# Kernel optimization log

Hardware: AMD Instinct MI355X
Metric: run time of the kernel (lower is better)

## Reference

```python
import jax, jax.numpy as jnp
import numpy as np

BATCH = 256
B_TYPES = 32   # input capsule types
C_TYPES = 10   # output capsule types
H, W = 8, 8    # input spatial extent == kernel (output is 1x1)
POSE = 16      # capsule pose length (shape (16,1))
NUM_ITER = 3
EPS = 1e-8


def setup_inputs() -> dict:
    key = jax.random.key(0)
    k1, k2, k3 = jax.random.split(key, 3)
    input_caps_poses = jax.random.normal(k1, (BATCH, B_TYPES, H, W, POSE, 1), jnp.float32)
    input_caps_activations = jax.random.uniform(k2, (BATCH, B_TYPES, H, W), jnp.float32)
    # nn.init.normal_(std=0.1) on [B, kh, kw, C, os0, is0]
    weight = 0.1 * jax.random.normal(k3, (B_TYPES, H, W, C_TYPES, POSE, POSE), jnp.float32)
    # routing_bias initialized to 0.1: [C, oh, ow, os0, os1]
    routing_bias = jnp.full((C_TYPES, 1, 1, POSE, 1), 0.1, jnp.float32)
    return {
        "input_caps_poses": input_caps_poses,
        "input_caps_activations": input_caps_activations,
        "weight": weight,
        "routing_bias": routing_bias,
    }


def _squash(s):
    # Hinton squash: ||s||^2/(1+||s||^2) * s/||s||, norm over pose dims
    n2 = jnp.sum(s * s, axis=(-2, -1), keepdims=True)
    return (n2 / (1.0 + n2)) * s * jax.lax.rsqrt(n2 + EPS)


def reference(input_caps_poses, input_caps_activations, weight, routing_bias):
    b = input_caps_poses.shape[0]
    # votes[b,c,B,h,w,o,p] = sum_i W[B,h,w,c,o,i] * pose[b,B,h,w,i,p]
    votes = jnp.einsum('Bhwcoi,bBhwip->bcBhwop', weight, input_caps_poses)
    logits = jnp.zeros((b, C_TYPES, B_TYPES, H, W), votes.dtype)
    bias = routing_bias.reshape(1, C_TYPES, POSE, 1)
    v = None
    for it in range(NUM_ITER):
        # coupling coefficients: softmax over output capsule types
        c = jax.nn.softmax(logits, axis=1)                      # [b,C,B,h,w]
        # weighted sum of votes over all input capsules (B,h,w)
        s = jnp.einsum('bcBhw,bcBhwop->bcop', c, votes) + bias  # [b,C,16,1]
        v = _squash(s)
        if it < NUM_ITER - 1:
            # agreement: dot(vote, output pose)
            logits = logits + jnp.einsum('bcBhwop,bcop->bcBhw', votes, v)
    output_caps_poses = v[:, :, None, None, :, :]               # [b,C,1,1,16,1]
    output_caps_activations = jnp.sqrt(
        jnp.sum(v * v, axis=(-2, -1)) + EPS)[:, :, None, None]  # [b,C,1,1]
    return output_caps_poses, output_caps_activations
```

## Files before the change

### kernel.cpp

```cpp
#include <hip/hip_runtime.h>
#include <hip/hip_fp16.h>
#include <math.h>


typedef _Float16 f16;
typedef _Float16 f16x2 __attribute__((ext_vector_type(2)));
typedef _Float16 f16x4 __attribute__((ext_vector_type(4)));
typedef _Float16 f16x8 __attribute__((ext_vector_type(8)));
typedef __fp16   h16x2 __attribute__((ext_vector_type(2)));
typedef float f32x4 __attribute__((ext_vector_type(4)));

#define DPP_ADD(v, ctrl) ((v) + __int_as_float(__builtin_amdgcn_update_dpp( \
    0, __float_as_int(v), (ctrl), 0xF, 0xF, true)))

__device__ __forceinline__ f16x2 pk(float a, float b) {
    h16x2 t = __builtin_amdgcn_cvt_pkrtz(a, b);
    return __builtin_bit_cast(f16x2, t);
}

#if __has_builtin(__builtin_amdgcn_fdot2)
__device__ __forceinline__ float FDOT2(f16x2 a, f16x2 b, float c) {
    return __builtin_amdgcn_fdot2(__builtin_bit_cast(h16x2, a),
                                  __builtin_bit_cast(h16x2, b), c, false);
}
#else
__device__ __forceinline__ float FDOT2(f16x2 a, f16x2 b, float c) {
    return c + (float)a[0] * (float)b[0] + (float)a[1] * (float)b[1];
}
#endif

constexpr int WS_ROW = 28;
constexpr int XS_ROW = 76;

__device__ __forceinline__ float xorsum4(float v) {
    v += __shfl_xor(v, 16, 64);
    v += __shfl_xor(v, 32, 64);
    return v;
}

__device__ __forceinline__ f16x4 cvt4(float4 w) {
    f16x2 a = pk(w.x, w.y);
    f16x2 b = pk(w.z, w.w);
    f16x4 r; r[0] = a[0]; r[1] = a[1]; r[2] = b[0]; r[3] = b[1];
    return r;
}

template<int PASS>
__global__ __launch_bounds__(256)
void pass_k(const float* __restrict__ poses, const float* __restrict__ weight,
            const float* __restrict__ bias,
            const float* __restrict__ sp0, const float* __restrict__ sp1,
            float* __restrict__ s_dst)
{
    __shared__ f16 Ws[640 * WS_ROW];
    __shared__ f16 xs[64 * XS_ROW];

    const int tid  = threadIdx.x;
    const int blk  = blockIdx.x;
    const int ngrp = blk >> 2;
    const int b0   = (blk & 3) * 64;
    const int wave = tid >> 6;
    const int lane = tid & 63;
    const int q    = lane >> 4;
    const int lo   = lane & 15;
    const int wtb  = wave * 16;
    const int bg   = b0 + wtb;
    const int nl0  = q >> 1;
    const int iq   = (q & 1) * 8;

    f16x2 vsp[10][2];
    if (PASS >= 1) {
        const int rowb = (bg + lo) * 10;
        #pragma unroll
        for (int c = 0; c < 10; ++c) {
            float4 bb = *(const float4*)(bias + c * 16 + q * 4);
            float4 sa = *(const float4*)(sp0 + (size_t)(rowb + c) * 16 + q * 4);
            float t0 = sa.x + bb.x, t1 = sa.y + bb.y, t2 = sa.z + bb.z, t3 = sa.w + bb.w;
            float n2 = xorsum4(t0*t0 + t1*t1 + t2*t2 + t3*t3);
            float sc = n2 / (1.f + n2) * rsqrtf(n2 + 1e-8f);
            float v0 = sc*t0, v1 = sc*t1, v2 = sc*t2, v3 = sc*t3;
            if (PASS == 2) {
                float4 sb = *(const float4*)(sp1 + (size_t)(rowb + c) * 16 + q * 4);
                float u0 = sb.x + bb.x, u1 = sb.y + bb.y, u2 = sb.z + bb.z, u3 = sb.w + bb.w;
                float m2 = xorsum4(u0*u0 + u1*u1 + u2*u2 + u3*u3);
                float sc2 = m2 / (1.f + m2) * rsqrtf(m2 + 1e-8f);
                v0 += sc2*u0; v1 += sc2*u1; v2 += sc2*u2; v3 += sc2*u3;
            }
            vsp[c][0] = pk(v0, v1);
            vsp[c][1] = pk(v2, v3);
        }
    }

    float4 wreg[10];
    float4 xreg[4];
    const int b_loc = tid >> 2, part = tid & 3;

    auto load_iter = [&](int l) {
        const float* wp = weight + (size_t)(ngrp * 4 + l) * 10240;
        #pragma unroll
        for (int k = 0; k < 10; ++k) wreg[k] = ((const float4*)wp)[tid + k * 256];
        const float* xp = poses + (size_t)(b0 + b_loc) * 32768
                          + (size_t)(ngrp * 16 + l * 4 + part) * 16;
        #pragma unroll
        for (int j = 0; j < 4; ++j) xreg[j] = ((const float4*)xp)[j];
    };
    auto store_iter = [&]() {
        #pragma unroll
        for (int k = 0; k < 10; ++k) {
            const int f = tid + k * 256;
            *(f16x4*)&Ws[(f >> 2) * WS_ROW + (f & 3) * 4] = cvt4(wreg[k]);
        }
        f16* lp = xs + b_loc * XS_ROW + part * 16;
        #pragma unroll
        for (int j = 0; j < 4; ++j) *(f16x4*)&lp[j * 4] = cvt4(xreg[j]);
    };

    f32x4 acc[10];
    #pragma unroll
    for (int c = 0; c < 10; ++c) acc[c] = (f32x4){0.f, 0.f, 0.f, 0.f};

    f16x2 cf[10][2];

    load_iter(0);

    for (int l = 0; l < 4; ++l) {
        __syncthreads();
        store_iter();
        if (l + 1 < 4) load_iter(l + 1);
        __syncthreads();

        if (PASS >= 1) {
            float ce[10];
            #pragma unroll
            for (int n = 0; n < 4; ++n) {
                f16x4 bx = *(const f16x4*)&xs[(wtb + lo) * XS_ROW + n * 16 + q * 4];
                float lg[10];
                #pragma unroll
                for (int c = 0; c < 10; ++c) {
                    f16x4 aw = *(const f16x4*)&Ws[((n * 10 + c) * 16 + lo) * WS_ROW + q * 4];
                    f32x4 D = __builtin_amdgcn_mfma_f32_16x16x16f16(
                        aw, bx, (f32x4){0.f, 0.f, 0.f, 0.f}, 0, 0, 0);
                    float p = FDOT2(pk(D[0], D[1]), vsp[c][0], 0.f);
                    p = FDOT2(pk(D[2], D[3]), vsp[c][1], p);
                    lg[c] = xorsum4(p);
                }
                float m = lg[0];
                #pragma unroll
                for (int c = 1; c < 10; ++c) m = fmaxf(m, lg[c]);
                float sum = 0.f;
                #pragma unroll
                for (int c = 0; c < 10; ++c) { lg[c] = __expf(lg[c] - m); sum += lg[c]; }
                const float inv = 1.f / sum;
                if (n & 1) {
                    #pragma unroll
                    for (int c = 0; c < 10; ++c)
                        cf[c][n >> 1] = pk(ce[c], lg[c] * inv);
                } else {
                    #pragma unroll
                    for (int c = 0; c < 10; ++c) ce[c] = lg[c] * inv;
                }
            }
        }

        f16x8 xa[2];
        #pragma unroll
        for (int np = 0; np < 2; ++np) {
            const f16* p = &xs[(wtb + lo) * XS_ROW + (np * 2 + nl0) * 16 + iq];
            f16x4 x0 = *(const f16x4*)p;
            f16x4 x1 = *(const f16x4*)(p + 4);
            xa[np] = __builtin_shufflevector(x0, x1, 0, 1, 2, 3, 4, 5, 6, 7);
        }
        #pragma unroll
        for (int c = 0; c < 10; ++c) {
            #pragma unroll
            for (int np = 0; np < 2; ++np) {
                f16 ch;
                if (PASS == 0) {
                    ch = (f16)0.1f;
                } else {
                    union { f16x2 h; unsigned u; } cu; cu.h = cf[c][np];
                    unsigned hv = nl0 ? (cu.u >> 16) : (cu.u & 0xffffu);
                    union { unsigned short s; f16 h; } hu; hu.s = (unsigned short)hv;
                    ch = hu.h;
                }
                const int n_loc = np * 2 + nl0;
                const f16* wp_ = &Ws[((n_loc * 10 + c) * 16 + lo) * WS_ROW + iq];
                f16x4 w0 = *(const f16x4*)wp_;
                f16x4 w1 = *(const f16x4*)(wp_ + 4);
                f16x8 bw = __builtin_shufflevector(w0, w1, 0, 1, 2, 3, 4, 5, 6, 7);
                f16x8 av = xa[np] * ch;
                acc[c] = __builtin_amdgcn_mfma_f32_16x16x32_f16(av, bw, acc[c], 0, 0, 0);
            }
        }
    }

    #pragma unroll
    for (int c = 0; c < 10; ++c) {
        float* sp = s_dst + ((size_t)(bg + q * 4) * 10 + c) * 16 + lo;
        unsafeAtomicAdd(sp + 0 * 160, acc[c][0]);
        unsafeAtomicAdd(sp + 1 * 160, acc[c][1]);
        unsafeAtomicAdd(sp + 2 * 160, acc[c][2]);
        unsafeAtomicAdd(sp + 3 * 160, acc[c][3]);
    }
}

__global__ __launch_bounds__(256)
void epi_k(const float* __restrict__ s2, const float* __restrict__ bias,
           float* __restrict__ out)
{
    const int t = blockIdx.x * 256 + threadIdx.x;
    if (t >= 2560) return;
    const int c = t % 10;
    const float* sp = s2 + (size_t)t * 16;
    const float* bp = bias + c * 16;
    float sv[16];
    float n2 = 0.f;
    #pragma unroll
    for (int o = 0; o < 16; ++o) { float v = sp[o] + bp[o]; sv[o] = v; n2 += v * v; }
    const float scale = n2 / (1.f + n2) * rsqrtf(n2 + 1e-8f);
    float a2 = 0.f;
    #pragma unroll
    for (int o = 0; o < 16; ++o) {
        float v = scale * sv[o];
        out[(size_t)t * 16 + o] = v;
        a2 += v * v;
    }
    out[40960 + t] = sqrtf(a2 + 1e-8f);
}

extern "C" void kernel_launch(void* const* d_in, const int* in_sizes, int n_in,
                              void* d_out, int out_size, void* d_ws, size_t ws_size,
                              hipStream_t stream)
{
    const float* poses  = (const float*)d_in[0];
    const float* weight = (const float*)d_in[2];
    const float* bias   = (const float*)d_in[3];
    float* out = (float*)d_out;
    float* s0 = (float*)d_ws;
    float* s1 = s0 + 40960;
    float* s2 = s1 + 40960;

    (void)hipMemsetAsync(d_ws, 0, 3 * 40960 * sizeof(float), stream);

    pass_k<0><<<512, 256, 0, stream>>>(poses, weight, bias, nullptr, nullptr, s0);
    pass_k<1><<<512, 256, 0, stream>>>(poses, weight, bias, s0, nullptr, s1);
    pass_k<2><<<512, 256, 0, stream>>>(poses, weight, bias, s0, s1, s2);
    epi_k<<<10, 256, 0, stream>>>(s2, bias, out);
}
```

Before: 204.7 us.

## Pre-convert inputs to fp16 once, widen blocks to 512 threads with in-block reduction

Adds a prep kernel that converts weights and poses to fp16 once, so the three routing passes read half the bytes and skip per-pass conversion. Each pass block now has 8 waves that split the spatial positions into two halves, with 16-byte LDS loads and new padding. The halves are summed through shared memory before the global atomics, which halves atomic traffic. In exchange it adds two extra kernel launches and a full fp16 copy of the inputs written and read through the workspace.

```diff
diff --git a/kernel.cpp b/kernel.cpp
--- a/kernel.cpp
+++ b/kernel.cpp
@@ -10,9 +10,6 @@
 typedef __fp16   h16x2 __attribute__((ext_vector_type(2)));
 typedef float f32x4 __attribute__((ext_vector_type(4)));
 
-#define DPP_ADD(v, ctrl) ((v) + __int_as_float(__builtin_amdgcn_update_dpp( \
-    0, __float_as_int(v), (ctrl), 0xF, 0xF, true)))
-
 __device__ __forceinline__ f16x2 pk(float a, float b) {
     h16x2 t = __builtin_amdgcn_cvt_pkrtz(a, b);
     return __builtin_bit_cast(f16x2, t);
@@ -29,8 +26,8 @@
 }
 #endif
 
-constexpr int WS_ROW = 28;
-constexpr int XS_ROW = 76;
+constexpr int WS_ROW = 24;
+constexpr int XS_ROW = 136;
 
 __device__ __forceinline__ float xorsum4(float v) {
     v += __shfl_xor(v, 16, 64);
@@ -38,21 +35,28 @@
     return v;
 }
 
-__device__ __forceinline__ f16x4 cvt4(float4 w) {
-    f16x2 a = pk(w.x, w.y);
-    f16x2 b = pk(w.z, w.w);
-    f16x4 r; r[0] = a[0]; r[1] = a[1]; r[2] = b[0]; r[3] = b[1];
-    return r;
+__global__ __launch_bounds__(256)
+void prep_k(const float* __restrict__ src, f16* __restrict__ dst, int npair)
+{
+    const int i = blockIdx.x * 256 + threadIdx.x;
+    if (i >= npair) return;
+    float4 a = ((const float4*)src)[2 * i];
+    float4 b = ((const float4*)src)[2 * i + 1];
+    f16x2 p0 = pk(a.x, a.y), p1 = pk(a.z, a.w), p2 = pk(b.x, b.y), p3 = pk(b.z, b.w);
+    f16x8 r;
+    r[0] = p0[0]; r[1] = p0[1]; r[2] = p1[0]; r[3] = p1[1];
+    r[4] = p2[0]; r[5] = p2[1]; r[6] = p3[0]; r[7] = p3[1];
+    *(f16x8*)&dst[(size_t)i * 8] = r;
 }
 
 template<int PASS>
-__global__ __launch_bounds__(256)
-void pass_k(const float* __restrict__ poses, const float* __restrict__ weight,
+__global__ __launch_bounds__(512, 4)
+void pass_k(const f16* __restrict__ x16, const f16* __restrict__ w16,
             const float* __restrict__ bias,
             const float* __restrict__ sp0, const float* __restrict__ sp1,
             float* __restrict__ s_dst)
 {
-    __shared__ f16 Ws[640 * WS_ROW];
+    __shared__ f16 Ws[1280 * WS_ROW];
     __shared__ f16 xs[64 * XS_ROW];
 
     const int tid  = threadIdx.x;
@@ -63,8 +67,11 @@
     const int lane = tid & 63;
     const int q    = lane >> 4;
     const int lo   = lane & 15;
-    const int wtb  = wave * 16;
+    const int t    = wave & 3;
+    const int h    = wave >> 2;
+    const int wtb  = t * 16;
     const int bg   = b0 + wtb;
+    const int hbase = h * 4;
     const int nl0  = q >> 1;
     const int iq   = (q & 1) * 8;
 
@@ -91,28 +98,29 @@
         }
     }
 
-    float4 wreg[10];
-    float4 xreg[4];
-    const int b_loc = tid >> 2, part = tid & 3;
+    f16x8 wreg[5];
+    f16x8 xreg[2];
+    const int b_loc = tid >> 3, part = tid & 7;
 
     auto load_iter = [&](int l) {
-        const float* wp = weight + (size_t)(ngrp * 4 + l) * 10240;
-        #pragma unroll
-        for (int k = 0; k < 10; ++k) wreg[k] = ((const float4*)wp)[tid + k * 256];
-        const float* xp = poses + (size_t)(b0 + b_loc) * 32768
-                          + (size_t)(ngrp * 16 + l * 4 + part) * 16;
-        #pragma unroll
-        for (int j = 0; j < 4; ++j) xreg[j] = ((const float4*)xp)[j];
+        const f16* wp = w16 + (size_t)(ngrp * 16 + l * 8) * 2560;
+        #pragma unroll
+        for (int k = 0; k < 5; ++k)
+            wreg[k] = ((const f16x8*)wp)[tid + k * 512];
+        const f16* xp = x16 + (size_t)(b0 + b_loc) * 32768
+                        + (size_t)(ngrp * 16 + l * 8 + part) * 16;
+        xreg[0] = ((const f16x8*)xp)[0];
+        xreg[1] = ((const f16x8*)xp)[1];
     };
     auto store_iter = [&]() {
         #pragma unroll
-        for (int k = 0; k < 10; ++k) {
-            const int f = tid + k * 256;
-            *(f16x4*)&Ws[(f >> 2) * WS_ROW + (f & 3) * 4] = cvt4(wreg[k]);
+        for (int k = 0; k < 5; ++k) {
+            const int f = tid + k * 512;
+            *(f16x8*)&Ws[(f >> 1) * WS_ROW + (f & 1) * 8] = wreg[k];
         }
         f16* lp = xs + b_loc * XS_ROW + part * 16;
-        #pragma unroll
-        for (int j = 0; j < 4; ++j) *(f16x4*)&lp[j * 4] = cvt4(xreg[j]);
+        *(f16x8*)&lp[0] = xreg[0];
+        *(f16x8*)&lp[8] = xreg[1];
     };
 
     f32x4 acc[10];
@@ -123,21 +131,22 @@
 
     load_iter(0);
 
-    for (int l = 0; l < 4; ++l) {
+    for (int l = 0; l < 2; ++l) {
         __syncthreads();
         store_iter();
-        if (l + 1 < 4) load_iter(l + 1);
+        if (l == 0) load_iter(1);
         __syncthreads();
 
         if (PASS >= 1) {
             float ce[10];
             #pragma unroll
             for (int n = 0; n < 4; ++n) {
-                f16x4 bx = *(const f16x4*)&xs[(wtb + lo) * XS_ROW + n * 16 + q * 4];
+                const int n8 = hbase + n;
+                f16x4 bx = *(const f16x4*)&xs[(wtb + lo) * XS_ROW + n8 * 16 + q * 4];
                 float lg[10];
                 #pragma unroll
                 for (int c = 0; c < 10; ++c) {
-                    f16x4 aw = *(const f16x4*)&Ws[((n * 10 + c) * 16 + lo) * WS_ROW + q * 4];
+                    f16x4 aw = *(const f16x4*)&Ws[((n8 * 10 + c) * 16 + lo) * WS_ROW + q * 4];
                     f32x4 D = __builtin_amdgcn_mfma_f32_16x16x16f16(
                         aw, bx, (f32x4){0.f, 0.f, 0.f, 0.f}, 0, 0, 0);
                     float p = FDOT2(pk(D[0], D[1]), vsp[c][0], 0.f);
@@ -153,8 +162,7 @@
                 const float inv = 1.f / sum;
                 if (n & 1) {
                     #pragma unroll
-                    for (int c = 0; c < 10; ++c)
-                        cf[c][n >> 1] = pk(ce[c], lg[c] * inv);
+                    for (int c = 0; c < 10; ++c) cf[c][n >> 1] = pk(ce[c], lg[c] * inv);
                 } else {
                     #pragma unroll
                     for (int c = 0; c < 10; ++c) ce[c] = lg[c] * inv;
@@ -164,12 +172,8 @@
 
         f16x8 xa[2];
         #pragma unroll
-        for (int np = 0; np < 2; ++np) {
-            const f16* p = &xs[(wtb + lo) * XS_ROW + (np * 2 + nl0) * 16 + iq];
-            f16x4 x0 = *(const f16x4*)p;
-            f16x4 x1 = *(const f16x4*)(p + 4);
-            xa[np] = __builtin_shufflevector(x0, x1, 0, 1, 2, 3, 4, 5, 6, 7);
-        }
+        for (int np = 0; np < 2; ++np)
+            xa[np] = *(const f16x8*)&xs[(wtb + lo) * XS_ROW + (hbase + np * 2 + nl0) * 16 + iq];
         #pragma unroll
         for (int c = 0; c < 10; ++c) {
             #pragma unroll
@@ -178,29 +182,38 @@
                 if (PASS == 0) {
                     ch = (f16)0.1f;
                 } else {
-                    union { f16x2 h; unsigned u; } cu; cu.h = cf[c][np];
+                    union { f16x2 h2; unsigned u; } cu; cu.h2 = cf[c][np];
                     unsigned hv = nl0 ? (cu.u >> 16) : (cu.u & 0xffffu);
-                    union { unsigned short s; f16 h; } hu; hu.s = (unsigned short)hv;
-                    ch = hu.h;
+                    union { unsigned short s; f16 hh; } hu; hu.s = (unsigned short)hv;
+                    ch = hu.hh;
                 }
-                const int n_loc = np * 2 + nl0;
-                const f16* wp_ = &Ws[((n_loc * 10 + c) * 16 + lo) * WS_ROW + iq];
-                f16x4 w0 = *(const f16x4*)wp_;
-                f16x4 w1 = *(const f16x4*)(wp_ + 4);
-                f16x8 bw = __builtin_shufflevector(w0, w1, 0, 1, 2, 3, 4, 5, 6, 7);
+                const int n8 = hbase + np * 2 + nl0;
+                f16x8 bw = *(const f16x8*)&Ws[((n8 * 10 + c) * 16 + lo) * WS_ROW + iq];
                 f16x8 av = xa[np] * ch;
                 acc[c] = __builtin_amdgcn_mfma_f32_16x16x32_f16(av, bw, acc[c], 0, 0, 0);
             }
         }
     }
 
-    #pragma unroll
-    for (int c = 0; c < 10; ++c) {
-        float* sp = s_dst + ((size_t)(bg + q * 4) * 10 + c) * 16 + lo;
-        unsafeAtomicAdd(sp + 0 * 160, acc[c][0]);
-        unsafeAtomicAdd(sp + 1 * 160, acc[c][1]);
-        unsafeAtomicAdd(sp + 2 * 160, acc[c][2]);
-        unsafeAtomicAdd(sp + 3 * 160, acc[c][3]);
+    __syncthreads();
+    float* xch = (float*)Ws;
+    if (h == 1) {
+        #pragma unroll
+        for (int c = 0; c < 10; ++c)
+            #pragma unroll
+            for (int r = 0; r < 4; ++r)
+                xch[((t * 16 + q * 4 + r) * 10 + c) * 17 + lo] = acc[c][r];
+    }
+    __syncthreads();
+    if (h == 0) {
+        #pragma unroll
+        for (int c = 0; c < 10; ++c) {
+            #pragma unroll
+            for (int r = 0; r < 4; ++r) {
+                float val = acc[c][r] + xch[((t * 16 + q * 4 + r) * 10 + c) * 17 + lo];
+                unsafeAtomicAdd(s_dst + ((size_t)(bg + q * 4 + r) * 10 + c) * 16 + lo, val);
+            }
+        }
     }
 }
 
@@ -236,14 +249,20 @@
     const float* weight = (const float*)d_in[2];
     const float* bias   = (const float*)d_in[3];
     float* out = (float*)d_out;
+
     float* s0 = (float*)d_ws;
     float* s1 = s0 + 40960;
     float* s2 = s1 + 40960;
+    f16*   w16 = (f16*)(s2 + 40960);
+    f16*   x16 = w16 + 5242880;
 
     (void)hipMemsetAsync(d_ws, 0, 3 * 40960 * sizeof(float), stream);
 
-    pass_k<0><<<512, 256, 0, stream>>>(poses, weight, bias, nullptr, nullptr, s0);
-    pass_k<1><<<512, 256, 0, stream>>>(poses, weight, bias, s0, nullptr, s1);
-    pass_k<2><<<512, 256, 0, stream>>>(poses, weight, bias, s0, s1, s2);
+    prep_k<<<2560, 256, 0, stream>>>(weight, w16, 655360);
+    prep_k<<<4096, 256, 0, stream>>>(poses,  x16, 1048576);
+
+    pass_k<0><<<512, 512, 0, stream>>>(x16, w16, bias, nullptr, nullptr, s0);
+    pass_k<1><<<512, 512, 0, stream>>>(x16, w16, bias, s0, nullptr, s1);
+    pass_k<2><<<512, 512, 0, stream>>>(x16, w16, bias, s0, s1, s2);
     epi_k<<<10, 256, 0, stream>>>(s2, bias, out);
 }
```

After: 293.3 us. 43.3% more time.

## Split capsule types across wave pairs and halve batch tile per block

Applied to the files above, without the earlier changes.

Each block now handles 32 batch rows instead of 64, and the four waves split into two batch halves times two groups of 5 output types. Logits are exchanged through a small shared buffer, with an extra barrier, so each wave can compute the full 10-way softmax. The grid doubles to 1024 blocks, and padding changes let the code use 8-wide LDS loads. The aim is more blocks and fewer registers per thread (launch bounds ask for 4 blocks per CU), at the cost of loading each weight tile twice as often and adding a sync.

```diff
diff --git a/kernel.cpp b/kernel.cpp
--- a/kernel.cpp
+++ b/kernel.cpp
@@ -10,9 +10,6 @@
 typedef __fp16   h16x2 __attribute__((ext_vector_type(2)));
 typedef float f32x4 __attribute__((ext_vector_type(4)));
 
-#define DPP_ADD(v, ctrl) ((v) + __int_as_float(__builtin_amdgcn_update_dpp( \
-    0, __float_as_int(v), (ctrl), 0xF, 0xF, true)))
-
 __device__ __forceinline__ f16x2 pk(float a, float b) {
     h16x2 t = __builtin_amdgcn_cvt_pkrtz(a, b);
     return __builtin_bit_cast(f16x2, t);
@@ -29,8 +26,9 @@
 }
 #endif
 
-constexpr int WS_ROW = 28;
-constexpr int XS_ROW = 76;
+constexpr int WS_ROW = 24;
+constexpr int XS_ROW = 72;
+constexpr int LG_ROW = 48;
 
 __device__ __forceinline__ float xorsum4(float v) {
     v += __shfl_xor(v, 16, 64);
@@ -46,33 +44,39 @@
 }
 
 template<int PASS>
-__global__ __launch_bounds__(256)
+__global__ __launch_bounds__(256, 4)
 void pass_k(const float* __restrict__ poses, const float* __restrict__ weight,
             const float* __restrict__ bias,
             const float* __restrict__ sp0, const float* __restrict__ sp1,
             float* __restrict__ s_dst)
 {
     __shared__ f16 Ws[640 * WS_ROW];
-    __shared__ f16 xs[64 * XS_ROW];
+    __shared__ f16 xs[32 * XS_ROW];
+    __shared__ f16 lgx[32 * LG_ROW];
 
     const int tid  = threadIdx.x;
     const int blk  = blockIdx.x;
-    const int ngrp = blk >> 2;
-    const int b0   = (blk & 3) * 64;
+    const int ngrp = blk >> 3;
+    const int b0   = (blk & 7) * 32;
     const int wave = tid >> 6;
     const int lane = tid & 63;
     const int q    = lane >> 4;
     const int lo   = lane & 15;
-    const int wtb  = wave * 16;
+    const int t    = wave & 1;
+    const int g    = wave >> 1;
+    const int c0   = g * 5;
+    const int go   = (1 - g) * 5;
+    const int wtb  = t * 16;
     const int bg   = b0 + wtb;
     const int nl0  = q >> 1;
     const int iq   = (q & 1) * 8;
 
-    f16x2 vsp[10][2];
+    f16x2 vsp[5][2];
     if (PASS >= 1) {
         const int rowb = (bg + lo) * 10;
         #pragma unroll
-        for (int c = 0; c < 10; ++c) {
+        for (int cc = 0; cc < 5; ++cc) {
+            const int c = c0 + cc;
             float4 bb = *(const float4*)(bias + c * 16 + q * 4);
             float4 sa = *(const float4*)(sp0 + (size_t)(rowb + c) * 16 + q * 4);
             float t0 = sa.x + bb.x, t1 = sa.y + bb.y, t2 = sa.z + bb.z, t3 = sa.w + bb.w;
@@ -86,23 +90,23 @@
                 float sc2 = m2 / (1.f + m2) * rsqrtf(m2 + 1e-8f);
                 v0 += sc2*u0; v1 += sc2*u1; v2 += sc2*u2; v3 += sc2*u3;
             }
-            vsp[c][0] = pk(v0, v1);
-            vsp[c][1] = pk(v2, v3);
+            vsp[cc][0] = pk(v0, v1);
+            vsp[cc][1] = pk(v2, v3);
         }
     }
 
     float4 wreg[10];
-    float4 xreg[4];
-    const int b_loc = tid >> 2, part = tid & 3;
+    float4 xreg[2];
+    const int b_loc = tid >> 3, part = tid & 7;
 
     auto load_iter = [&](int l) {
         const float* wp = weight + (size_t)(ngrp * 4 + l) * 10240;
         #pragma unroll
         for (int k = 0; k < 10; ++k) wreg[k] = ((const float4*)wp)[tid + k * 256];
         const float* xp = poses + (size_t)(b0 + b_loc) * 32768
-                          + (size_t)(ngrp * 16 + l * 4 + part) * 16;
-        #pragma unroll
-        for (int j = 0; j < 4; ++j) xreg[j] = ((const float4*)xp)[j];
+                          + (size_t)(ngrp * 16 + l * 4) * 16 + part * 8;
+        xreg[0] = ((const float4*)xp)[0];
+        xreg[1] = ((const float4*)xp)[1];
     };
     auto store_iter = [&]() {
         #pragma unroll
@@ -110,16 +114,17 @@
             const int f = tid + k * 256;
             *(f16x4*)&Ws[(f >> 2) * WS_ROW + (f & 3) * 4] = cvt4(wreg[k]);
         }
-        f16* lp = xs + b_loc * XS_ROW + part * 16;
-        #pragma unroll
-        for (int j = 0; j < 4; ++j) *(f16x4*)&lp[j * 4] = cvt4(xreg[j]);
+        f16x4 r0 = cvt4(xreg[0]), r1 = cvt4(xreg[1]);
+        f16x8 r = __builtin_shufflevector(r0, r1, 0, 1, 2, 3, 4, 5, 6, 7);
+        *(f16x8*)&xs[b_loc * XS_ROW + part * 8] = r;
     };
 
-    f32x4 acc[10];
-    #pragma unroll
-    for (int c = 0; c < 10; ++c) acc[c] = (f32x4){0.f, 0.f, 0.f, 0.f};
-
-    f16x2 cf[10][2];
+    f32x4 acc[5];
+    #pragma unroll
+    for (int cc = 0; cc < 5; ++cc) acc[cc] = (f32x4){0.f, 0.f, 0.f, 0.f};
+
+    f16x2 cf[5][2];
+    float lgs[4][5];
 
     load_iter(0);
 
@@ -130,77 +135,90 @@
         __syncthreads();
 
         if (PASS >= 1) {
-            float ce[10];
             #pragma unroll
             for (int n = 0; n < 4; ++n) {
                 f16x4 bx = *(const f16x4*)&xs[(wtb + lo) * XS_ROW + n * 16 + q * 4];
-                float lg[10];
-                #pragma unroll
-                for (int c = 0; c < 10; ++c) {
-                    f16x4 aw = *(const f16x4*)&Ws[((n * 10 + c) * 16 + lo) * WS_ROW + q * 4];
+                #pragma unroll
+                for (int cc = 0; cc < 5; ++cc) {
+                    f16x4 aw = *(const f16x4*)&Ws[((n * 10 + c0 + cc) * 16 + lo) * WS_ROW + q * 4];
                     f32x4 D = __builtin_amdgcn_mfma_f32_16x16x16f16(
                         aw, bx, (f32x4){0.f, 0.f, 0.f, 0.f}, 0, 0, 0);
-                    float p = FDOT2(pk(D[0], D[1]), vsp[c][0], 0.f);
-                    p = FDOT2(pk(D[2], D[3]), vsp[c][1], p);
-                    lg[c] = xorsum4(p);
-                }
-                float m = lg[0];
-                #pragma unroll
-                for (int c = 1; c < 10; ++c) m = fmaxf(m, lg[c]);
+                    float p = FDOT2(pk(D[0], D[1]), vsp[cc][0], 0.f);
+                    p = FDOT2(pk(D[2], D[3]), vsp[cc][1], p);
+                    lgs[n][cc] = xorsum4(p);
+                }
+                if (q == 0) {
+                    #pragma unroll
+                    for (int cc = 0; cc < 5; ++cc)
+                        lgx[(wtb + lo) * LG_ROW + n * 12 + c0 + cc] = (f16)lgs[n][cc];
+                }
+            }
+            __syncthreads();
+
+            #pragma unroll
+            for (int n = 0; n < 4; ++n) {
+                float pf[5];
+                #pragma unroll
+                for (int cc = 0; cc < 5; ++cc)
+                    pf[cc] = (float)lgx[(wtb + lo) * LG_ROW + n * 12 + go + cc];
+                float m = lgs[n][0];
+                #pragma unroll
+                for (int cc = 1; cc < 5; ++cc) m = fmaxf(m, lgs[n][cc]);
+                #pragma unroll
+                for (int cc = 0; cc < 5; ++cc) m = fmaxf(m, pf[cc]);
                 float sum = 0.f;
-                #pragma unroll
-                for (int c = 0; c < 10; ++c) { lg[c] = __expf(lg[c] - m); sum += lg[c]; }
+                float eo[5];
+                #pragma unroll
+                for (int cc = 0; cc < 5; ++cc) { eo[cc] = __expf(lgs[n][cc] - m); sum += eo[cc]; }
+                #pragma unroll
+                for (int cc = 0; cc < 5; ++cc) sum += __expf(pf[cc] - m);
                 const float inv = 1.f / sum;
                 if (n & 1) {
                     #pragma unroll
-                    for (int c = 0; c < 10; ++c)
-                        cf[c][n >> 1] = pk(ce[c], lg[c] * inv);
+                    for (int cc = 0; cc < 5; ++cc)
+                        cf[cc][n >> 1][1] = (f16)(eo[cc] * inv);
                 } else {
                     #pragma unroll
-                    for (int c = 0; c < 10; ++c) ce[c] = lg[c] * inv;
+                    for (int cc = 0; cc < 5; ++cc) {
+                        f16x2 z; z[0] = (f16)(eo[cc] * inv); z[1] = (f16)0.f;
+                        cf[cc][n >> 1] = z;
+                    }
                 }
             }
         }
 
         f16x8 xa[2];
         #pragma unroll
-        for (int np = 0; np < 2; ++np) {
-            const f16* p = &xs[(wtb + lo) * XS_ROW + (np * 2 + nl0) * 16 + iq];
-            f16x4 x0 = *(const f16x4*)p;
-            f16x4 x1 = *(const f16x4*)(p + 4);
-            xa[np] = __builtin_shufflevector(x0, x1, 0, 1, 2, 3, 4, 5, 6, 7);
-        }
-        #pragma unroll
-        for (int c = 0; c < 10; ++c) {
+        for (int np = 0; np < 2; ++np)
+            xa[np] = *(const f16x8*)&xs[(wtb + lo) * XS_ROW + (np * 2 + nl0) * 16 + iq];
+        #pragma unroll
+        for (int cc = 0; cc < 5; ++cc) {
             #pragma unroll
             for (int np = 0; np < 2; ++np) {
                 f16 ch;
                 if (PASS == 0) {
                     ch = (f16)0.1f;
                 } else {
-                    union { f16x2 h; unsigned u; } cu; cu.h = cf[c][np];
+                    union { f16x2 h2; unsigned u; } cu; cu.h2 = cf[cc][np];
                     unsigned hv = nl0 ? (cu.u >> 16) : (cu.u & 0xffffu);
-                    union { unsigned short s; f16 h; } hu; hu.s = (unsigned short)hv;
-                    ch = hu.h;
+                    union { unsigned short s; f16 hh; } hu; hu.s = (unsigned short)hv;
+                    ch = hu.hh;
                 }
                 const int n_loc = np * 2 + nl0;
-                const f16* wp_ = &Ws[((n_loc * 10 + c) * 16 + lo) * WS_ROW + iq];
-                f16x4 w0 = *(const f16x4*)wp_;
-                f16x4 w1 = *(const f16x4*)(wp_ + 4);
-                f16x8 bw = __builtin_shufflevector(w0, w1, 0, 1, 2, 3, 4, 5, 6, 7);
+                f16x8 bw = *(const f16x8*)&Ws[((n_loc * 10 + c0 + cc) * 16 + lo) * WS_ROW + iq];
                 f16x8 av = xa[np] * ch;
-                acc[c] = __builtin_amdgcn_mfma_f32_16x16x32_f16(av, bw, acc[c], 0, 0, 0);
-            }
-        }
-    }
-
-    #pragma unroll
-    for (int c = 0; c < 10; ++c) {
-        float* sp = s_dst + ((size_t)(bg + q * 4) * 10 + c) * 16 + lo;
-        unsafeAtomicAdd(sp + 0 * 160, acc[c][0]);
-        unsafeAtomicAdd(sp + 1 * 160, acc[c][1]);
-        unsafeAtomicAdd(sp + 2 * 160, acc[c][2]);
-        unsafeAtomicAdd(sp + 3 * 160, acc[c][3]);
+                acc[cc] = __builtin_amdgcn_mfma_f32_16x16x32_f16(av, bw, acc[cc], 0, 0, 0);
+            }
+        }
+    }
+
+    #pragma unroll
+    for (int cc = 0; cc < 5; ++cc) {
+        float* sp = s_dst + ((size_t)(bg + q * 4) * 10 + c0 + cc) * 16 + lo;
+        unsafeAtomicAdd(sp + 0 * 160, acc[cc][0]);
+        unsafeAtomicAdd(sp + 1 * 160, acc[cc][1]);
+        unsafeAtomicAdd(sp + 2 * 160, acc[cc][2]);
+        unsafeAtomicAdd(sp + 3 * 160, acc[cc][3]);
     }
 }
 
@@ -242,8 +260,8 @@
 
     (void)hipMemsetAsync(d_ws, 0, 3 * 40960 * sizeof(float), stream);
 
-    pass_k<0><<<512, 256, 0, stream>>>(poses, weight, bias, nullptr, nullptr, s0);
-    pass_k<1><<<512, 256, 0, stream>>>(poses, weight, bias, s0, nullptr, s1);
-    pass_k<2><<<512, 256, 0, stream>>>(poses, weight, bias, s0, s1, s2);
+    pass_k<0><<<1024, 256, 0, stream>>>(poses, weight, bias, nullptr, nullptr, s0);
+    pass_k<1><<<1024, 256, 0, stream>>>(poses, weight, bias, s0, nullptr, s1);
+    pass_k<2><<<1024, 256, 0, stream>>>(poses, weight, bias, s0, s1, s2);
     epi_k<<<10, 256, 0, stream>>>(s2, bias, out);
 }
```

Measured after the change: 299.8 us. +46.5%, slower.

## Halve per-block spatial work, double grid, widen LDS loads to 16 bytes

Applied to the files above, without the earlier changes.

Each block now processes 8 spatial positions in two staged iterations instead of 16 in four, and the grid doubles to 1024 blocks per pass. This gives more parallelism across the CUs, and launch bounds now request 4 blocks per CU. LDS row pitches drop to 24/72 halfs so MFMA operands can be read as single 16-byte f16x8 loads instead of two 8-byte loads. In exchange there are twice as many atomic adds into the s buffers, and the new padding may cause LDS bank conflicts.

```diff
diff --git a/kernel.cpp b/kernel.cpp
--- a/kernel.cpp
+++ b/kernel.cpp
@@ -10,9 +10,6 @@
 typedef __fp16   h16x2 __attribute__((ext_vector_type(2)));
 typedef float f32x4 __attribute__((ext_vector_type(4)));
 
-#define DPP_ADD(v, ctrl) ((v) + __int_as_float(__builtin_amdgcn_update_dpp( \
-    0, __float_as_int(v), (ctrl), 0xF, 0xF, true)))
-
 __device__ __forceinline__ f16x2 pk(float a, float b) {
     h16x2 t = __builtin_amdgcn_cvt_pkrtz(a, b);
     return __builtin_bit_cast(f16x2, t);
@@ -29,8 +26,8 @@
 }
 #endif
 
-constexpr int WS_ROW = 28;
-constexpr int XS_ROW = 76;
+constexpr int WS_ROW = 24;
+constexpr int XS_ROW = 72;
 
 __device__ __forceinline__ float xorsum4(float v) {
     v += __shfl_xor(v, 16, 64);
@@ -46,7 +43,7 @@
 }
 
 template<int PASS>
-__global__ __launch_bounds__(256)
+__global__ __launch_bounds__(256, 4)
 void pass_k(const float* __restrict__ poses, const float* __restrict__ weight,
             const float* __restrict__ bias,
             const float* __restrict__ sp0, const float* __restrict__ sp1,
@@ -96,11 +93,11 @@
     const int b_loc = tid >> 2, part = tid & 3;
 
     auto load_iter = [&](int l) {
-        const float* wp = weight + (size_t)(ngrp * 4 + l) * 10240;
+        const float* wp = weight + (size_t)(ngrp * 8 + l * 4) * 2560;
         #pragma unroll
         for (int k = 0; k < 10; ++k) wreg[k] = ((const float4*)wp)[tid + k * 256];
         const float* xp = poses + (size_t)(b0 + b_loc) * 32768
-                          + (size_t)(ngrp * 16 + l * 4 + part) * 16;
+                          + (size_t)(ngrp * 8 + l * 4 + part) * 16;
         #pragma unroll
         for (int j = 0; j < 4; ++j) xreg[j] = ((const float4*)xp)[j];
     };
@@ -123,10 +120,10 @@
 
     load_iter(0);
 
-    for (int l = 0; l < 4; ++l) {
+    for (int l = 0; l < 2; ++l) {
         __syncthreads();
         store_iter();
-        if (l + 1 < 4) load_iter(l + 1);
+        if (l == 0) load_iter(1);
         __syncthreads();
 
         if (PASS >= 1) {
@@ -153,8 +150,7 @@
                 const float inv = 1.f / sum;
                 if (n & 1) {
                     #pragma unroll
-                    for (int c = 0; c < 10; ++c)
-                        cf[c][n >> 1] = pk(ce[c], lg[c] * inv);
+                    for (int c = 0; c < 10; ++c) cf[c][n >> 1] = pk(ce[c], lg[c] * inv);
                 } else {
                     #pragma unroll
                     for (int c = 0; c < 10; ++c) ce[c] = lg[c] * inv;
@@ -164,12 +160,8 @@
 
         f16x8 xa[2];
         #pragma unroll
-        for (int np = 0; np < 2; ++np) {
-            const f16* p = &xs[(wtb + lo) * XS_ROW + (np * 2 + nl0) * 16 + iq];
-            f16x4 x0 = *(const f16x4*)p;
-            f16x4 x1 = *(const f16x4*)(p + 4);
-            xa[np] = __builtin_shufflevector(x0, x1, 0, 1, 2, 3, 4, 5, 6, 7);
-        }
+        for (int np = 0; np < 2; ++np)
+            xa[np] = *(const f16x8*)&xs[(wtb + lo) * XS_ROW + (np * 2 + nl0) * 16 + iq];
         #pragma unroll
         for (int c = 0; c < 10; ++c) {
             #pragma unroll
@@ -178,16 +170,13 @@
                 if (PASS == 0) {
                     ch = (f16)0.1f;
                 } else {
-                    union { f16x2 h; unsigned u; } cu; cu.h = cf[c][np];
+                    union { f16x2 h2; unsigned u; } cu; cu.h2 = cf[c][np];
                     unsigned hv = nl0 ? (cu.u >> 16) : (cu.u & 0xffffu);
-                    union { unsigned short s; f16 h; } hu; hu.s = (unsigned short)hv;
-                    ch = hu.h;
+                    union { unsigned short s; f16 hh; } hu; hu.s = (unsigned short)hv;
+                    ch = hu.hh;
                 }
                 const int n_loc = np * 2 + nl0;
-                const f16* wp_ = &Ws[((n_loc * 10 + c) * 16 + lo) * WS_ROW + iq];
-                f16x4 w0 = *(const f16x4*)wp_;
-                f16x4 w1 = *(const f16x4*)(wp_ + 4);
-                f16x8 bw = __builtin_shufflevector(w0, w1, 0, 1, 2, 3, 4, 5, 6, 7);
+                f16x8 bw = *(const f16x8*)&Ws[((n_loc * 10 + c) * 16 + lo) * WS_ROW + iq];
                 f16x8 av = xa[np] * ch;
                 acc[c] = __builtin_amdgcn_mfma_f32_16x16x32_f16(av, bw, acc[c], 0, 0, 0);
             }
@@ -242,8 +231,8 @@
 
     (void)hipMemsetAsync(d_ws, 0, 3 * 40960 * sizeof(float), stream);
 
-    pass_k<0><<<512, 256, 0, stream>>>(poses, weight, bias, nullptr, nullptr, s0);
-    pass_k<1><<<512, 256, 0, stream>>>(poses, weight, bias, s0, nullptr, s1);
-    pass_k<2><<<512, 256, 0, stream>>>(poses, weight, bias, s0, s1, s2);
+    pass_k<0><<<1024, 256, 0, stream>>>(poses, weight, bias, nullptr, nullptr, s0);
+    pass_k<1><<<1024, 256, 0, stream>>>(poses, weight, bias, s0, nullptr, s1);
+    pass_k<2><<<1024, 256, 0, stream>>>(poses, weight, bias, s0, s1, s2);
     epi_k<<<10, 256, 0, stream>>>(s2, bias, out);
 }
```

After: 321.5 us. 1.57x slower.
